# Kernel tuning notes

Measured on AMD Instinct MI355X. Metric: run time of the kernel, lower is better.

The kernel has to match this reference:

```python
import jax, jax.numpy as jnp
import numpy as np

jax.config.update("jax_enable_x64", True)

VOCAB_R_MAX = 3.0
EPS = 1e-8


def _sanitize(x):
    # torch.nan_to_num(x, nan=0.0, posinf=10000.0, neginf=-10000.0)
    return jnp.nan_to_num(x, nan=0.0, posinf=10000.0, neginf=-10000.0)


def setup_inputs() -> dict:
    key = jax.random.key(0)
    k1, k2 = jax.random.split(key, 2)
    B, L, V, n = 2, 512, 50257, 768
    hidden_states = jax.random.normal(k1, (B, L, n + 1), dtype=jnp.float32)
    # nn.Parameter(torch.randn(V, n) * 0.01) -- tangent vectors
    weight = jax.random.normal(k2, (V, n), dtype=jnp.float32) * 0.01
    # init_temp = 1/sqrt(n_embd)
    logit_scale = jnp.asarray(1.0 / np.sqrt(n), dtype=jnp.float32)
    return {"hidden_states": hidden_states, "weight": weight, "logit_scale": logit_scale}


def _exp_map_zero(v_spatial, max_tangent_norm):
    # Lorentz exp map at origin (curvature -1), tangent vector (0, v_spatial).
    # Norm is clamped to max_tangent_norm (geodesic radius ceiling).
    r = jnp.linalg.norm(v_spatial, axis=-1, keepdims=True)  # [V,1]
    rc = jnp.minimum(r, max_tangent_norm)
    dirv = v_spatial / jnp.maximum(r, EPS)
    return jnp.concatenate([jnp.cosh(rc), jnp.sinh(rc) * dirv], axis=-1)  # [V, n+1]


def _ensure_lorentz(x):
    # Project onto the hyperboloid: x0 = sqrt(1 + ||x_spatial||^2)
    sp = x[..., 1:]
    t = jnp.sqrt(1.0 + jnp.sum(sp * sp, axis=-1, keepdims=True))
    return jnp.concatenate([t, sp], axis=-1)


def reference(hidden_states, weight, logit_scale):
    x = _ensure_lorentz(_sanitize(hidden_states))          # [B,L,n+1]
    w = _sanitize(_exp_map_zero(weight, VOCAB_R_MAX))       # [V,n+1]

    x64 = x.astype(jnp.float64)
    w64 = w.astype(jnp.float64)
    # Minkowski inner product split into time/space einsums (as in source)
    time_inner = jnp.einsum('blt,vt->blv', x64[..., :1], w64[:, :1])
    space_inner = jnp.einsum('bls,vs->blv', x64[..., 1:], w64[:, 1:])
    inner = space_inner - time_inner                        # [B,L,V] fp64

    tau = jnp.clip(logit_scale, 0.01, 2.5).astype(jnp.float64)
    logits = (inner * tau).astype(hidden_states.dtype)
    return _sanitize(logits)
```

## Files before the change

kernel.cpp:

```cpp
#include <hip/hip_runtime.h>
#include <hip/hip_bf16.h>
#include <cstdint>
#include <cstddef>

typedef __attribute__((ext_vector_type(4))) float f32x4;
typedef __attribute__((ext_vector_type(8))) short bf16x8;
typedef unsigned short ushort_t;

#define KDIM 768
#define BM 128
#define BN 128
#define BK 64
#define NKT 12

static __device__ __forceinline__ float sani(float x) {
  if (__builtin_isnan(x)) return 0.0f;
  if (__builtin_isinf(x)) return x > 0.0f ? 1.0e4f : -1.0e4f;
  return x;
}

static __device__ __forceinline__ unsigned short f2bf(float x) {
  unsigned u = __builtin_bit_cast(unsigned, x);
  unsigned r = 0x7FFFu + ((u >> 16) & 1u);
  return (unsigned short)((u + r) >> 16);
}


__global__ __launch_bounds__(256) void prep_x_kernel(
    const float* __restrict__ h, ushort_t* __restrict__ xl,
    float* __restrict__ tx) {
  const int row = blockIdx.x;
  const int t = threadIdx.x;
  const int swz = (row & 7) << 3;
  const float* src = h + (size_t)row * (KDIM + 1) + 1;
  float v0 = sani(src[t]);
  float v1 = sani(src[t + 256]);
  float v2 = sani(src[t + 512]);
  float ss = v0 * v0 + v1 * v1 + v2 * v2;
#pragma unroll
  for (int off = 32; off > 0; off >>= 1) ss += __shfl_down(ss, off);
  __shared__ float red[4];
  if ((t & 63) == 0) red[t >> 6] = ss;
  __syncthreads();
  if (t == 0) {
    float total = red[0] + red[1] + red[2] + red[3];
    tx[row] = sqrtf(1.0f + total);
  }
  ushort_t* dst = xl + (size_t)row * KDIM;
  dst[t ^ swz]         = f2bf(v0);
  dst[(t + 256) ^ swz] = f2bf(v1);
  dst[(t + 512) ^ swz] = f2bf(v2);
}

__global__ __launch_bounds__(256) void prep_w_kernel(
    const float* __restrict__ w, ushort_t* __restrict__ wl,
    float* __restrict__ cw, int V) {
  const int row = blockIdx.x;
  const int t = threadIdx.x;
  const int swz = (row & 7) << 3;
  ushort_t* dst = wl + (size_t)row * KDIM;
  if (row >= V) {
    dst[t] = 0; dst[t + 256] = 0; dst[t + 512] = 0;
    if (t == 0) cw[row] = 0.0f;
    return;
  }
  const float* src = w + (size_t)row * KDIM;
  float v0 = src[t];
  float v1 = src[t + 256];
  float v2 = src[t + 512];
  float ss = v0 * v0 + v1 * v1 + v2 * v2;
#pragma unroll
  for (int off = 32; off > 0; off >>= 1) ss += __shfl_down(ss, off);
  __shared__ float red[4];
  if ((t & 63) == 0) red[t >> 6] = ss;
  __syncthreads();
  float total = red[0] + red[1] + red[2] + red[3];
  float r = sqrtf(total);
  float rc = fminf(r, 3.0f);
  float sc = sinhf(rc) / fmaxf(r, 1e-8f);
  dst[t ^ swz]         = f2bf(sani(v0 * sc));
  dst[(t + 256) ^ swz] = f2bf(sani(v1 * sc));
  dst[(t + 512) ^ swz] = f2bf(sani(v2 * sc));
  if (t == 0) cw[row] = sani(coshf(rc));
}

#define GLD16(gp, sp)                                               \
  __builtin_amdgcn_global_load_lds(                                 \
      (const __attribute__((address_space(1))) void*)(gp),          \
      (__attribute__((address_space(3))) void*)(sp), 16, 0, 0)

__global__ __launch_bounds__(256) void gemm_kernel(
    const ushort_t* __restrict__ xl, const ushort_t* __restrict__ wl,
    const float* __restrict__ tx, const float* __restrict__ cw,
    const float* __restrict__ ls, float* __restrict__ out,
    int V, int Mtiles, int nwg8) {
  __shared__ ushort_t As[2][BM * BK];
  __shared__ ushort_t Bs[2][BN * BK];

  const int tid = threadIdx.x;
  const int lane = tid & 63;
  const int wid = tid >> 6;
  const int wr = wid >> 1;
  const int wc = wid & 1;

  const int g = blockIdx.x;
  const int L = (g & 7) * nwg8 + (g >> 3);
  const int bm = L & (Mtiles - 1);
  const int bn = L / Mtiles;

  const int l15 = lane & 15;
  const int lq = lane >> 4;
  const int srow = lane >> 3;
  const int scol = (lane & 7) * 8;
  const int swz = (l15 & 7) << 3;

  f32x4 acc[4][4];
#pragma unroll
  for (int i = 0; i < 4; ++i)
#pragma unroll
    for (int j = 0; j < 4; ++j) acc[i][j] = (f32x4){0.f, 0.f, 0.f, 0.f};

  const size_t a_row0 = (size_t)bm * BM;
  const size_t b_row0 = (size_t)bn * BN;

#define STAGE(B_, T_)                                                         \
  _Pragma("unroll") for (int c = 0; c < 4; ++c) {                             \
    const int chunk = wid * 4 + c;                                            \
    const int row = chunk * 8 + srow;                                         \
    GLD16(xl + (a_row0 + row) * KDIM + (T_) * BK + scol,                      \
          &As[B_][chunk * 512]);                                              \
    GLD16(wl + (b_row0 + row) * KDIM + (T_) * BK + scol,                      \
          &Bs[B_][chunk * 512]);                                              \
  }

#define COMPUTE(B_)                                                           \
  _Pragma("unroll") for (int kk = 0; kk < 2; ++kk) {                          \
    const int koff = (kk * 32 + lq * 8) ^ swz;                                \
    bf16x8 af[4], bfr[4];                                                     \
    _Pragma("unroll") for (int mi = 0; mi < 4; ++mi)                          \
        af[mi] =                                                              \
            *(const bf16x8*)&As[B_][(wr * 64 + mi * 16 + l15) * BK + koff];   \
    _Pragma("unroll") for (int ni = 0; ni < 4; ++ni)                          \
        bfr[ni] =                                                             \
            *(const bf16x8*)&Bs[B_][(wc * 64 + ni * 16 + l15) * BK + koff];   \
    _Pragma("unroll") for (int mi = 0; mi < 4; ++mi)                          \
      _Pragma("unroll") for (int ni = 0; ni < 4; ++ni)                        \
          acc[mi][ni] = __builtin_amdgcn_mfma_f32_16x16x32_bf16(              \
              bfr[ni], af[mi], acc[mi][ni], 0, 0, 0);                         \
  }

  STAGE(0, 0);
  asm volatile("s_waitcnt vmcnt(0)" ::: "memory");
  __builtin_amdgcn_s_barrier();

#pragma unroll 2
  for (int t = 0; t < NKT; ++t) {
    const int cur = t & 1;
    if (t + 1 < NKT) STAGE(cur ^ 1, t + 1);
    __builtin_amdgcn_sched_barrier(0);
    COMPUTE(cur);
    __builtin_amdgcn_sched_barrier(0);
    asm volatile("s_waitcnt vmcnt(0)" ::: "memory");
    __builtin_amdgcn_s_barrier();
  }

  float tau = ls[0];
  tau = fminf(fmaxf(tau, 0.01f), 2.5f);

#pragma unroll
  for (int mi = 0; mi < 4; ++mi) {
    const int mg = (int)a_row0 + wr * 64 + mi * 16 + l15;
    const float txm = tx[mg];
    float* orow = out + (size_t)mg * V;
#pragma unroll
    for (int ni = 0; ni < 4; ++ni) {
      const int nb = (int)b_row0 + wc * 64 + ni * 16 + lq * 4;
      const f32x4 cw4 = *(const f32x4*)&cw[nb];
      f32x4 v;
#pragma unroll
      for (int j = 0; j < 4; ++j)
        v[j] = (acc[mi][ni][j] - txm * cw4[j]) * tau;
      if (nb + 3 < V) {
        __builtin_memcpy(&orow[nb], &v, 16);
      } else {
#pragma unroll
        for (int j = 0; j < 4; ++j)
          if (nb + j < V) orow[nb + j] = v[j];
      }
    }
  }
#undef STAGE
#undef COMPUTE
}

extern "C" void kernel_launch(void* const* d_in, const int* in_sizes, int n_in,
                              void* d_out, int out_size, void* d_ws, size_t ws_size,
                              hipStream_t stream) {
  const float* h = (const float*)d_in[0];
  const float* w = (const float*)d_in[1];
  const float* ls = (const float*)d_in[2];
  float* out = (float*)d_out;

  const int M = in_sizes[0] / (KDIM + 1);
  const int V = in_sizes[1] / KDIM;
  const int Vpad = (V + BN - 1) & ~(BN - 1);

  char* ws = (char*)d_ws;
  ushort_t* wl = (ushort_t*)ws;
  ushort_t* xl = (ushort_t*)(ws + (size_t)Vpad * KDIM * 2);
  float* cw = (float*)(ws + (size_t)Vpad * KDIM * 2 + (size_t)M * KDIM * 2);
  float* tx = cw + Vpad;

  prep_x_kernel<<<dim3(M), dim3(256), 0, stream>>>(h, xl, tx);
  prep_w_kernel<<<dim3(Vpad), dim3(256), 0, stream>>>(w, wl, cw, V);

  const int Mtiles = M / BM;
  const int nwg = Mtiles * (Vpad / BN);
  gemm_kernel<<<dim3(nwg), dim3(256), 0, stream>>>(
      xl, wl, tx, cw, ls, out, V, Mtiles, nwg / 8);
}
```

Before: 212.5 us.

## Triple-buffer GEMM with BK=32 and XOR swizzle applied at LDS staging

```diff
diff --git a/kernel.cpp b/kernel.cpp
--- a/kernel.cpp
+++ b/kernel.cpp
@@ -10,8 +10,8 @@
 #define KDIM 768
 #define BM 128
 #define BN 128
-#define BK 64
-#define NKT 12
+#define BK 32
+#define NKT 24
 
 static __device__ __forceinline__ float sani(float x) {
   if (__builtin_isnan(x)) return 0.0f;
@@ -31,7 +31,6 @@
     float* __restrict__ tx) {
   const int row = blockIdx.x;
   const int t = threadIdx.x;
-  const int swz = (row & 7) << 3;
   const float* src = h + (size_t)row * (KDIM + 1) + 1;
   float v0 = sani(src[t]);
   float v1 = sani(src[t + 256]);
@@ -47,9 +46,9 @@
     tx[row] = sqrtf(1.0f + total);
   }
   ushort_t* dst = xl + (size_t)row * KDIM;
-  dst[t ^ swz]         = f2bf(v0);
-  dst[(t + 256) ^ swz] = f2bf(v1);
-  dst[(t + 512) ^ swz] = f2bf(v2);
+  dst[t]       = f2bf(v0);
+  dst[t + 256] = f2bf(v1);
+  dst[t + 512] = f2bf(v2);
 }
 
 __global__ __launch_bounds__(256) void prep_w_kernel(
@@ -57,7 +56,6 @@
     float* __restrict__ cw, int V) {
   const int row = blockIdx.x;
   const int t = threadIdx.x;
-  const int swz = (row & 7) << 3;
   ushort_t* dst = wl + (size_t)row * KDIM;
   if (row >= V) {
     dst[t] = 0; dst[t + 256] = 0; dst[t + 512] = 0;
@@ -78,9 +76,9 @@
   float r = sqrtf(total);
   float rc = fminf(r, 3.0f);
   float sc = sinhf(rc) / fmaxf(r, 1e-8f);
-  dst[t ^ swz]         = f2bf(sani(v0 * sc));
-  dst[(t + 256) ^ swz] = f2bf(sani(v1 * sc));
-  dst[(t + 512) ^ swz] = f2bf(sani(v2 * sc));
+  dst[t]       = f2bf(sani(v0 * sc));
+  dst[t + 256] = f2bf(sani(v1 * sc));
+  dst[t + 512] = f2bf(sani(v2 * sc));
   if (t == 0) cw[row] = sani(coshf(rc));
 }
 
@@ -89,13 +87,12 @@
       (const __attribute__((address_space(1))) void*)(gp),          \
       (__attribute__((address_space(3))) void*)(sp), 16, 0, 0)
 
-__global__ __launch_bounds__(256) void gemm_kernel(
+__global__ __launch_bounds__(256, 2) void gemm_kernel(
     const ushort_t* __restrict__ xl, const ushort_t* __restrict__ wl,
     const float* __restrict__ tx, const float* __restrict__ cw,
     const float* __restrict__ ls, float* __restrict__ out,
     int V, int Mtiles, int nwg8) {
-  __shared__ ushort_t As[2][BM * BK];
-  __shared__ ushort_t Bs[2][BN * BK];
+  __shared__ ushort_t lds[3 * 8192];
 
   const int tid = threadIdx.x;
   const int lane = tid & 63;
@@ -110,9 +107,22 @@
 
   const int l15 = lane & 15;
   const int lq = lane >> 4;
-  const int srow = lane >> 3;
-  const int scol = (lane & 7) * 8;
-  const int swz = (l15 & 7) << 3;
+
+  const int a_row0 = bm * BM;
+  const int b_row0 = bn * BN;
+
+  const int ggl = (lane & 7) ^ (lane >> 3);
+  const int rl = 2 * (lane >> 3) + (ggl >> 2);
+  const int cg = (ggl & 3) * 8;
+  const size_t axs0 = (size_t)(a_row0 + 16 * wid + rl) * KDIM + cg;
+  const size_t axs1 = (size_t)(a_row0 + 16 * (wid + 4) + rl) * KDIM + cg;
+  const size_t bxs0 = (size_t)(b_row0 + 16 * wid + rl) * KDIM + cg;
+  const size_t bxs1 = (size_t)(b_row0 + 16 * (wid + 4) + rl) * KDIM + cg;
+
+  const int rphys = l15 >> 1;
+  const int gph = (((l15 & 1) << 2) + lq) ^ rphys;
+  const int aoff = wr * 2048 + rphys * 64 + gph * 8;
+  const int boff = 4096 + wc * 2048 + rphys * 64 + gph * 8;
 
   f32x4 acc[4][4];
 #pragma unroll
@@ -120,61 +130,71 @@
 #pragma unroll
     for (int j = 0; j < 4; ++j) acc[i][j] = (f32x4){0.f, 0.f, 0.f, 0.f};
 
-  const size_t a_row0 = (size_t)bm * BM;
-  const size_t b_row0 = (size_t)bn * BN;
-
-#define STAGE(B_, T_)                                                         \
-  _Pragma("unroll") for (int c = 0; c < 4; ++c) {                             \
-    const int chunk = wid * 4 + c;                                            \
-    const int row = chunk * 8 + srow;                                         \
-    GLD16(xl + (a_row0 + row) * KDIM + (T_) * BK + scol,                      \
-          &As[B_][chunk * 512]);                                              \
-    GLD16(wl + (b_row0 + row) * KDIM + (T_) * BK + scol,                      \
-          &Bs[B_][chunk * 512]);                                              \
-  }
-
-#define COMPUTE(B_)                                                           \
-  _Pragma("unroll") for (int kk = 0; kk < 2; ++kk) {                          \
-    const int koff = (kk * 32 + lq * 8) ^ swz;                                \
-    bf16x8 af[4], bfr[4];                                                     \
+#define STAGE(T_, S_)                                                         \
+  {                                                                           \
+    GLD16(xl + axs0 + (T_) * BK, &lds[(S_) * 8192 + wid * 512]);              \
+    GLD16(xl + axs1 + (T_) * BK, &lds[(S_) * 8192 + (wid + 4) * 512]);        \
+    GLD16(wl + bxs0 + (T_) * BK, &lds[(S_) * 8192 + 4096 + wid * 512]);       \
+    GLD16(wl + bxs1 + (T_) * BK, &lds[(S_) * 8192 + 4096 + (wid + 4) * 512]); \
+  }
+
+#define COMPUTE(S_)                                                           \
+  {                                                                           \
+    bf16x8 af[4], bf[4];                                                      \
     _Pragma("unroll") for (int mi = 0; mi < 4; ++mi)                          \
-        af[mi] =                                                              \
-            *(const bf16x8*)&As[B_][(wr * 64 + mi * 16 + l15) * BK + koff];   \
+        af[mi] = *(const bf16x8*)&lds[(S_) * 8192 + aoff + mi * 512];         \
     _Pragma("unroll") for (int ni = 0; ni < 4; ++ni)                          \
-        bfr[ni] =                                                             \
-            *(const bf16x8*)&Bs[B_][(wc * 64 + ni * 16 + l15) * BK + koff];   \
+        bf[ni] = *(const bf16x8*)&lds[(S_) * 8192 + boff + ni * 512];         \
+    asm volatile("s_waitcnt lgkmcnt(0)" ::: "memory");                        \
+    __builtin_amdgcn_sched_barrier(0);                                        \
+    __builtin_amdgcn_s_barrier();     \
+    __builtin_amdgcn_s_setprio(1);                                            \
     _Pragma("unroll") for (int mi = 0; mi < 4; ++mi)                          \
       _Pragma("unroll") for (int ni = 0; ni < 4; ++ni)                        \
           acc[mi][ni] = __builtin_amdgcn_mfma_f32_16x16x32_bf16(              \
-              bfr[ni], af[mi], acc[mi][ni], 0, 0, 0);                         \
+              bf[ni], af[mi], acc[mi][ni], 0, 0, 0);                          \
+    __builtin_amdgcn_s_setprio(0);                                            \
+  }
+
+#define BODY(T_, S_, SN_)                                                     \
+  {                                                                           \
+    STAGE((T_) + 2, SN_);                                                     \
+    asm volatile("s_waitcnt vmcnt(8)" ::: "memory");                          \
+    __builtin_amdgcn_s_barrier();                                             \
+    COMPUTE(S_);                                                              \
   }
 
   STAGE(0, 0);
+  STAGE(1, 1);
+
+#pragma unroll 1
+  for (int tt = 0; tt < 7; ++tt) {
+    const int t3 = tt * 3;
+    BODY(t3 + 0, 0, 2);
+    BODY(t3 + 1, 1, 0);
+    BODY(t3 + 2, 2, 1);
+  }
+  BODY(21, 0, 2);
+  asm volatile("s_waitcnt vmcnt(4)" ::: "memory");
+  __builtin_amdgcn_s_barrier();
+  COMPUTE(1);
   asm volatile("s_waitcnt vmcnt(0)" ::: "memory");
   __builtin_amdgcn_s_barrier();
-
-#pragma unroll 2
-  for (int t = 0; t < NKT; ++t) {
-    const int cur = t & 1;
-    if (t + 1 < NKT) STAGE(cur ^ 1, t + 1);
-    __builtin_amdgcn_sched_barrier(0);
-    COMPUTE(cur);
-    __builtin_amdgcn_sched_barrier(0);
-    asm volatile("s_waitcnt vmcnt(0)" ::: "memory");
-    __builtin_amdgcn_s_barrier();
-  }
+  COMPUTE(2);
+
+  asm volatile("" ::: "memory");
 
   float tau = ls[0];
   tau = fminf(fmaxf(tau, 0.01f), 2.5f);
 
 #pragma unroll
   for (int mi = 0; mi < 4; ++mi) {
-    const int mg = (int)a_row0 + wr * 64 + mi * 16 + l15;
+    const int mg = a_row0 + wr * 64 + mi * 16 + l15;
     const float txm = tx[mg];
     float* orow = out + (size_t)mg * V;
 #pragma unroll
     for (int ni = 0; ni < 4; ++ni) {
-      const int nb = (int)b_row0 + wc * 64 + ni * 16 + lq * 4;
+      const int nb = b_row0 + wc * 64 + ni * 16 + lq * 4;
       const f32x4 cw4 = *(const f32x4*)&cw[nb];
       f32x4 v;
 #pragma unroll
@@ -191,6 +211,7 @@
   }
 #undef STAGE
 #undef COMPUTE
+#undef BODY
 }
 
 extern "C" void kernel_launch(void* const* d_in, const int* in_sizes, int n_in,
```

Result: faster. 190.4 us (-10.4%).
